# Kernel optimization log

Hardware: AMD Instinct MI355X
Metric: run time of the kernel (lower is better)

## Reference

```python
import jax, jax.numpy as jnp
import numpy as np

VOCAB, E, H = 32000, 256, 256
B, T = 64, 2048


def setup_inputs() -> dict:
    key = jax.random.key(0)
    ks = jax.random.split(key, 6)
    X = jax.random.randint(ks[0], (B, T), 0, VOCAB)
    emb = jax.random.normal(ks[1], (VOCAB, E), dtype=jnp.float32)
    W_qrnn = jax.random.normal(ks[2], (E, 3 * H), dtype=jnp.float32) / np.sqrt(E)
    b_qrnn = jnp.zeros((3 * H,), dtype=jnp.float32)
    c0 = jax.random.normal(ks[3], (B, H), dtype=jnp.float32)
    W_out = jax.random.normal(ks[4], (H, 1), dtype=jnp.float32) / np.sqrt(H)
    b_out = jnp.zeros((1,), dtype=jnp.float32)
    return {"X": X, "emb": emb, "W_qrnn": W_qrnn, "b_qrnn": b_qrnn,
            "c0": c0, "W_out": W_out, "b_out": b_out}


def reference(X, emb, W_qrnn, b_qrnn, c0, W_out, b_out):
    # Embedding lookup: [B,T] -> [B,T,E]; permute to seq-major [T,B,E]
    x = jnp.transpose(emb[X], (1, 0, 2))
    # QRNN window=1 gate projection: all timesteps in one GEMM, [T,B,3H]
    g = jnp.einsum('tbe,ef->tbf', x, W_qrnn) + b_qrnn
    z, f, o = jnp.split(g, 3, axis=-1)
    z = jnp.tanh(z)
    f = jax.nn.sigmoid(f)
    o = jax.nn.sigmoid(o)

    # fo-pooling recurrence: c_t = f_t * c_{t-1} + (1 - f_t) * z_t
    def step(c, zf):
        z_t, f_t = zf
        c = f_t * c + (1.0 - f_t) * z_t
        return c, c

    _, cs = jax.lax.scan(step, c0, (z, f))  # cs: [T,B,H]
    h = o * cs                              # h_t = o_t * c_t
    hn = h[-1]                              # last timestep, [B,H]
    return hn @ W_out + b_out               # [B,1]
```

## Files before the change

kernel.cpp:

```cpp
#include <hip/hip_runtime.h>
#include <hip/hip_bf16.h>
#include <math.h>

#define EDIM 256
#define HDIM 256
#define BDIM 64
#define TDIM 2048
#define NC   64
#define TC   32

typedef __attribute__((ext_vector_type(8)))  short  short8;
typedef __attribute__((ext_vector_type(4)))  float  floatx4;
typedef __attribute__((ext_vector_type(4)))  unsigned int uintx4;

__device__ __forceinline__ unsigned short f2bf(float f) {
    unsigned int u = __float_as_uint(f);
    u += 0x7FFFu + ((u >> 16) & 1u);
    return (unsigned short)(u >> 16);
}
__device__ __forceinline__ unsigned int pk2(float a, float b) {
    return (unsigned int)f2bf(a) | ((unsigned int)f2bf(b) << 16);
}
__device__ __forceinline__ float sigm(float x) {
    return __builtin_amdgcn_rcpf(1.f + __expf(-x));
}
__device__ __forceinline__ float tanh_fast(float x) {
    return fmaf(-2.f, __builtin_amdgcn_rcpf(1.f + __expf(2.f * x)), 1.f);
}

__global__ __launch_bounds__(256) void conv_wp(const float* __restrict__ Wq,
                                               unsigned short* __restrict__ Wp) {
    const int bx = blockIdx.x;
    const int nt = (bx >> 3) & 7;
    const int hg = bx >> 6;
    const int ks = bx & 7;
    const int t = threadIdx.x;
    const int lane = t >> 2, pj = t & 3;
    const int col = lane & 15, q = lane >> 4;
    const int h = hg * 64 + (nt & 3) * 16 + col;
    const int c = (nt < 4) ? h : (HDIM + h);
    const int k = ks * 32 + q * 8 + pj * 2;
    unsigned int v = pk2(Wq[k * (3 * HDIM) + c], Wq[(k + 1) * (3 * HDIM) + c]);
    *(unsigned int*)(Wp + (size_t)bx * 512 + lane * 8 + pj * 2) = v;
}

__global__ __launch_bounds__(256) void conv_emb(const float* __restrict__ emb,
                                                unsigned short* __restrict__ ebf) {
    size_t i = ((size_t)blockIdx.x * 256 + threadIdx.x) * 8;
    floatx4 a = *(const floatx4*)(emb + i);
    floatx4 b = *(const floatx4*)(emb + i + 4);
    uintx4 o = {pk2(a.x, a.y), pk2(a.z, a.w), pk2(b.x, b.y), pk2(b.z, b.w)};
    *(uintx4*)(ebf + i) = o;
}

template<bool EMBBF>
__global__ __launch_bounds__(256, 2) void qrnn_mfma(
    const int* __restrict__ X, const float* __restrict__ emb,
    const unsigned short* __restrict__ ebf, const unsigned short* __restrict__ Wp,
    const float* __restrict__ bq, float* __restrict__ wsA, float* __restrict__ wsB)
{
    __shared__ __align__(16) short Bs[32768];

    const int tid = threadIdx.x;
    const int chunk = blockIdx.x, bg = blockIdx.y, hg = blockIdx.z;
    const int lane = tid & 63, w = tid >> 6;
    const int col = lane & 15, q = lane >> 4;
    const int t0 = chunk * TC;

    const unsigned short* wpb = Wp + (size_t)hg * 64 * 512;
#pragma unroll
    for (int i = 0; i < 16; ++i) {
        const int ch = w * 16 + i;
        __builtin_amdgcn_global_load_lds(
            (const __attribute__((address_space(1))) unsigned int*)(wpb + ch * 512 + lane * 8),
            (__attribute__((address_space(3))) unsigned int*)(Bs + ch * 512),
            16, 0, 0);
    }

    const int b0 = bg * 8 + 2 * w;
    int xid[4];
#pragma unroll
    for (int mt = 0; mt < 4; ++mt)
        xid[mt] = X[(b0 + (mt >> 1)) * TDIM + t0 + (mt & 1) * 16 + col];

    const unsigned short* ap[4];
    const float* apf[4];
#pragma unroll
    for (int mt = 0; mt < 4; ++mt) {
        if constexpr (EMBBF) ap[mt]  = ebf + (size_t)xid[mt] * EDIM + q * 8;
        else                 apf[mt] = emb + (size_t)xid[mt] * EDIM + q * 8;
    }

    floatx4 acc[4][8];
#pragma unroll
    for (int mt = 0; mt < 4; ++mt)
#pragma unroll
        for (int nt = 0; nt < 8; ++nt) acc[mt][nt] = (floatx4){0.f, 0.f, 0.f, 0.f};

    __syncthreads();

#pragma unroll
    for (int ks = 0; ks < 8; ++ks) {
        short8 af[4];
#pragma unroll
        for (int mt = 0; mt < 4; ++mt) {
            if constexpr (EMBBF) {
                af[mt] = *(const short8*)(ap[mt] + ks * 32);
            } else {
                floatx4 f0 = *(const floatx4*)(apf[mt] + ks * 32);
                floatx4 f1 = *(const floatx4*)(apf[mt] + ks * 32 + 4);
                uintx4 p = {pk2(f0.x, f0.y), pk2(f0.z, f0.w),
                            pk2(f1.x, f1.y), pk2(f1.z, f1.w)};
                af[mt] = *(short8*)&p;
            }
        }
        short8 bf[8];
#pragma unroll
        for (int nt = 0; nt < 8; ++nt)
            bf[nt] = *(const short8*)(Bs + (nt * 8 + ks) * 512 + lane * 8);
#pragma unroll
        for (int nt = 0; nt < 8; ++nt)
#pragma unroll
            for (int mt = 0; mt < 4; ++mt)
                acc[mt][nt] = __builtin_amdgcn_mfma_f32_16x16x32_bf16(af[mt], bf[nt], acc[mt][nt], 0, 0, 0);
    }

    const int hbase = hg * 64;
    float bz[4], bff[4];
#pragma unroll
    for (int nt = 0; nt < 4; ++nt) {
        bz[nt]  = bq[hbase + nt * 16 + col];
        bff[nt] = bq[HDIM + hbase + nt * 16 + col];
    }

    float Af0[4], Bf0[4], Af1[4], Bf1[4];
#pragma unroll
    for (int nt = 0; nt < 4; ++nt) {
        float Aseg[4], Bseg[4];
#pragma unroll
        for (int mt = 0; mt < 4; ++mt) {
            float Ac = 1.f, Bc = 0.f;
#pragma unroll
            for (int j = 0; j < 4; ++j) {
                float z = tanh_fast(acc[mt][nt][j] + bz[nt]);
                float f = sigm(acc[mt][nt + 4][j] + bff[nt]);
                Ac = f * Ac;
                Bc = fmaf(f, Bc, (1.f - f) * z);
            }
            Aseg[mt] = Ac; Bseg[mt] = Bc;
        }
#pragma unroll
        for (int s = 0; s < 2; ++s) {
            const int msk = 16 << s;
            const bool self_earlier = ((q >> s) & 1) == 0;
#pragma unroll
            for (int mt = 0; mt < 4; ++mt) {
                float Ap = __shfl_xor(Aseg[mt], msk, 64);
                float Bp = __shfl_xor(Bseg[mt], msk, 64);
                Bseg[mt] = self_earlier ? fmaf(Ap, Bseg[mt], Bp)
                                        : fmaf(Aseg[mt], Bp, Bseg[mt]);
                Aseg[mt] = Aseg[mt] * Ap;
            }
        }
        Af0[nt] = Aseg[0] * Aseg[1];
        Bf0[nt] = fmaf(Aseg[1], Bseg[0], Bseg[1]);
        Af1[nt] = Aseg[2] * Aseg[3];
        Bf1[nt] = fmaf(Aseg[3], Bseg[2], Bseg[3]);
    }

    float As0 = (q == 0) ? Af0[0] : (q == 1) ? Af0[1] : (q == 2) ? Af0[2] : Af0[3];
    float Bs0 = (q == 0) ? Bf0[0] : (q == 1) ? Bf0[1] : (q == 2) ? Bf0[2] : Bf0[3];
    float As1 = (q == 0) ? Af1[0] : (q == 1) ? Af1[1] : (q == 2) ? Af1[2] : Af1[3];
    float Bs1 = (q == 0) ? Bf1[0] : (q == 1) ? Bf1[1] : (q == 2) ? Bf1[2] : Bf1[3];

    const size_t r0 = ((size_t)chunk * BDIM + b0) * HDIM + hbase + lane;
    wsA[r0] = As0;          wsB[r0] = Bs0;
    wsA[r0 + HDIM] = As1;   wsB[r0 + HDIM] = Bs1;
}

__global__ __launch_bounds__(256) void qrnn_combine(
    const float* __restrict__ wsA, const float* __restrict__ wsB,
    const float* __restrict__ c0, const int* __restrict__ X,
    const float* __restrict__ emb, const float* __restrict__ Wq,
    const float* __restrict__ bq, const float* __restrict__ Wout,
    const float* __restrict__ bout, float* __restrict__ out)
{
    const int b = blockIdx.x;
    const int h = threadIdx.x;

    float c = c0[b * HDIM + h];
    for (int c8 = 0; c8 < NC; c8 += 8) {
        float a[8], bb[8];
#pragma unroll
        for (int i = 0; i < 8; ++i) {
            size_t base = ((size_t)(c8 + i) * BDIM + b) * HDIM + h;
            a[i]  = wsA[base];
            bb[i] = wsB[base];
        }
#pragma unroll
        for (int i = 0; i < 8; ++i) c = fmaf(a[i], c, bb[i]);
    }

    __shared__ float xs[EDIM];
    int idx = X[b * TDIM + (TDIM - 1)];
    xs[h] = emb[(size_t)idx * EDIM + h];
    __syncthreads();

    float acc = 0.f;
#pragma unroll 16
    for (int e = 0; e < EDIM; ++e)
        acc = fmaf(xs[e], Wq[e * (3 * HDIM) + 2 * HDIM + h], acc);

    float o  = 1.f / (1.f + expf(-(acc + bq[2 * HDIM + h])));
    float hn = o * c;

    __shared__ float red[HDIM];
    red[h] = hn * Wout[h];
    __syncthreads();
    for (int s = HDIM / 2; s > 0; s >>= 1) {
        if (h < s) red[h] += red[h + s];
        __syncthreads();
    }
    if (h == 0) out[b] = red[0] + bout[0];
}

extern "C" void kernel_launch(void* const* d_in, const int* in_sizes, int n_in,
                              void* d_out, int out_size, void* d_ws, size_t ws_size,
                              hipStream_t stream) {
    const int*   X    = (const int*)d_in[0];
    const float* emb  = (const float*)d_in[1];
    const float* Wq   = (const float*)d_in[2];
    const float* bq   = (const float*)d_in[3];
    const float* c0   = (const float*)d_in[4];
    const float* Wout = (const float*)d_in[5];
    const float* bout = (const float*)d_in[6];
    float* out = (float*)d_out;

    float* wsA = (float*)d_ws;
    float* wsB = wsA + (size_t)NC * BDIM * HDIM;
    unsigned short* Wp  = (unsigned short*)(wsB + (size_t)NC * BDIM * HDIM);
    unsigned short* ebf = Wp + (size_t)256 * 512;

    const size_t need_full = (size_t)2 * NC * BDIM * HDIM * 4
                           + (size_t)256 * 512 * 2
                           + (size_t)32000 * EDIM * 2;
    const bool full = ws_size >= need_full;

    conv_wp<<<256, 256, 0, stream>>>(Wq, Wp);
    if (full)
        conv_emb<<<(32000 * EDIM / 8) / 256, 256, 0, stream>>>(emb, ebf);

    dim3 g(NC, BDIM / 8, HDIM / 64);
    if (full) qrnn_mfma<true ><<<g, 256, 0, stream>>>(X, emb, ebf, Wp, bq, wsA, wsB);
    else      qrnn_mfma<false><<<g, 256, 0, stream>>>(X, emb, ebf, Wp, bq, wsA, wsB);

    qrnn_combine<<<BDIM, 256, 0, stream>>>(wsA, wsB, c0, X, emb, Wq, bq, Wout, bout, out);
}
```

Measured before the change: 169.4 us.

## Process multiple time chunks per block with prefetched A fragments and merged pack kernel

New measurement: 150.0 us. 11.5% less time.

```diff
diff --git a/kernel.cpp b/kernel.cpp
--- a/kernel.cpp
+++ b/kernel.cpp
@@ -8,6 +8,7 @@
 #define TDIM 2048
 #define NC   64
 #define TC   32
+#define CPB  4
 
 typedef __attribute__((ext_vector_type(8)))  short  short8;
 typedef __attribute__((ext_vector_type(4)))  float  floatx4;
@@ -28,29 +29,30 @@
     return fmaf(-2.f, __builtin_amdgcn_rcpf(1.f + __expf(2.f * x)), 1.f);
 }
 
-__global__ __launch_bounds__(256) void conv_wp(const float* __restrict__ Wq,
-                                               unsigned short* __restrict__ Wp) {
+__global__ __launch_bounds__(256) void qrnn_pack(
+    const float* __restrict__ Wq, const float* __restrict__ emb,
+    unsigned short* __restrict__ Wp, unsigned short* __restrict__ ebf)
+{
     const int bx = blockIdx.x;
-    const int nt = (bx >> 3) & 7;
-    const int hg = bx >> 6;
-    const int ks = bx & 7;
-    const int t = threadIdx.x;
-    const int lane = t >> 2, pj = t & 3;
-    const int col = lane & 15, q = lane >> 4;
-    const int h = hg * 64 + (nt & 3) * 16 + col;
-    const int c = (nt < 4) ? h : (HDIM + h);
-    const int k = ks * 32 + q * 8 + pj * 2;
-    unsigned int v = pk2(Wq[k * (3 * HDIM) + c], Wq[(k + 1) * (3 * HDIM) + c]);
-    *(unsigned int*)(Wp + (size_t)bx * 512 + lane * 8 + pj * 2) = v;
-}
-
-__global__ __launch_bounds__(256) void conv_emb(const float* __restrict__ emb,
-                                                unsigned short* __restrict__ ebf) {
-    size_t i = ((size_t)blockIdx.x * 256 + threadIdx.x) * 8;
-    floatx4 a = *(const floatx4*)(emb + i);
-    floatx4 b = *(const floatx4*)(emb + i + 4);
-    uintx4 o = {pk2(a.x, a.y), pk2(a.z, a.w), pk2(b.x, b.y), pk2(b.z, b.w)};
-    *(uintx4*)(ebf + i) = o;
+    if (bx < 256) {
+        const int nt = (bx >> 3) & 7;
+        const int hg = bx >> 6;
+        const int ks = bx & 7;
+        const int t = threadIdx.x;
+        const int lane = t >> 2, pj = t & 3;
+        const int col = lane & 15, q = lane >> 4;
+        const int h = hg * 64 + (nt & 3) * 16 + col;
+        const int c = (nt < 4) ? h : (HDIM + h);
+        const int k = ks * 32 + q * 8 + pj * 2;
+        unsigned int v = pk2(Wq[k * (3 * HDIM) + c], Wq[(k + 1) * (3 * HDIM) + c]);
+        *(unsigned int*)(Wp + (size_t)bx * 512 + lane * 8 + pj * 2) = v;
+    } else {
+        size_t i = ((size_t)(bx - 256) * 256 + threadIdx.x) * 8;
+        floatx4 a = *(const floatx4*)(emb + i);
+        floatx4 b = *(const floatx4*)(emb + i + 4);
+        uintx4 o = {pk2(a.x, a.y), pk2(a.z, a.w), pk2(b.x, b.y), pk2(b.z, b.w)};
+        *(uintx4*)(ebf + i) = o;
+    }
 }
 
 template<bool EMBBF>
@@ -59,71 +61,30 @@
     const unsigned short* __restrict__ ebf, const unsigned short* __restrict__ Wp,
     const float* __restrict__ bq, float* __restrict__ wsA, float* __restrict__ wsB)
 {
-    __shared__ __align__(16) short Bs[32768];
+    __shared__ __align__(16) short Bsh[32768];
 
     const int tid = threadIdx.x;
-    const int chunk = blockIdx.x, bg = blockIdx.y, hg = blockIdx.z;
+    const int cg = blockIdx.x, bg = blockIdx.y, hg = blockIdx.z;
     const int lane = tid & 63, w = tid >> 6;
     const int col = lane & 15, q = lane >> 4;
-    const int t0 = chunk * TC;
-
-    const unsigned short* wpb = Wp + (size_t)hg * 64 * 512;
+
+    const unsigned short* wpb = Wp + (size_t)hg * 32768;
 #pragma unroll
     for (int i = 0; i < 16; ++i) {
         const int ch = w * 16 + i;
         __builtin_amdgcn_global_load_lds(
             (const __attribute__((address_space(1))) unsigned int*)(wpb + ch * 512 + lane * 8),
-            (__attribute__((address_space(3))) unsigned int*)(Bs + ch * 512),
+            (__attribute__((address_space(3))) unsigned int*)(Bsh + ch * 512),
             16, 0, 0);
     }
 
     const int b0 = bg * 8 + 2 * w;
-    int xid[4];
-#pragma unroll
-    for (int mt = 0; mt < 4; ++mt)
-        xid[mt] = X[(b0 + (mt >> 1)) * TDIM + t0 + (mt & 1) * 16 + col];
-
-    const unsigned short* ap[4];
-    const float* apf[4];
-#pragma unroll
-    for (int mt = 0; mt < 4; ++mt) {
-        if constexpr (EMBBF) ap[mt]  = ebf + (size_t)xid[mt] * EDIM + q * 8;
-        else                 apf[mt] = emb + (size_t)xid[mt] * EDIM + q * 8;
-    }
-
-    floatx4 acc[4][8];
-#pragma unroll
-    for (int mt = 0; mt < 4; ++mt)
-#pragma unroll
-        for (int nt = 0; nt < 8; ++nt) acc[mt][nt] = (floatx4){0.f, 0.f, 0.f, 0.f};
-
-    __syncthreads();
-
-#pragma unroll
-    for (int ks = 0; ks < 8; ++ks) {
-        short8 af[4];
-#pragma unroll
-        for (int mt = 0; mt < 4; ++mt) {
-            if constexpr (EMBBF) {
-                af[mt] = *(const short8*)(ap[mt] + ks * 32);
-            } else {
-                floatx4 f0 = *(const floatx4*)(apf[mt] + ks * 32);
-                floatx4 f1 = *(const floatx4*)(apf[mt] + ks * 32 + 4);
-                uintx4 p = {pk2(f0.x, f0.y), pk2(f0.z, f0.w),
-                            pk2(f1.x, f1.y), pk2(f1.z, f1.w)};
-                af[mt] = *(short8*)&p;
-            }
-        }
-        short8 bf[8];
-#pragma unroll
-        for (int nt = 0; nt < 8; ++nt)
-            bf[nt] = *(const short8*)(Bs + (nt * 8 + ks) * 512 + lane * 8);
-#pragma unroll
-        for (int nt = 0; nt < 8; ++nt)
-#pragma unroll
-            for (int mt = 0; mt < 4; ++mt)
-                acc[mt][nt] = __builtin_amdgcn_mfma_f32_16x16x32_bf16(af[mt], bf[nt], acc[mt][nt], 0, 0, 0);
-    }
+    int xid[CPB][4];
+#pragma unroll
+    for (int c = 0; c < CPB; ++c)
+#pragma unroll
+        for (int mt = 0; mt < 4; ++mt)
+            xid[c][mt] = X[(b0 + (mt >> 1)) * TDIM + (cg * CPB + c) * TC + (mt & 1) * 16 + col];
 
     const int hbase = hg * 64;
     float bz[4], bff[4];
@@ -133,49 +94,102 @@
         bff[nt] = bq[HDIM + hbase + nt * 16 + col];
     }
 
-    float Af0[4], Bf0[4], Af1[4], Bf1[4];
-#pragma unroll
-    for (int nt = 0; nt < 4; ++nt) {
-        float Aseg[4], Bseg[4];
+    short8 abuf[3][4];
+    auto fetchA = [&](int c, int ks, int slot) {
 #pragma unroll
         for (int mt = 0; mt < 4; ++mt) {
-            float Ac = 1.f, Bc = 0.f;
-#pragma unroll
-            for (int j = 0; j < 4; ++j) {
-                float z = tanh_fast(acc[mt][nt][j] + bz[nt]);
-                float f = sigm(acc[mt][nt + 4][j] + bff[nt]);
-                Ac = f * Ac;
-                Bc = fmaf(f, Bc, (1.f - f) * z);
+            if constexpr (EMBBF) {
+                abuf[slot][mt] = *(const short8*)(ebf + (size_t)xid[c][mt] * EDIM + q * 8 + ks * 32);
+            } else {
+                const float* ap = emb + (size_t)xid[c][mt] * EDIM + q * 8 + ks * 32;
+                floatx4 f0 = *(const floatx4*)ap;
+                floatx4 f1 = *(const floatx4*)(ap + 4);
+                uintx4 p = {pk2(f0.x, f0.y), pk2(f0.z, f0.w),
+                            pk2(f1.x, f1.y), pk2(f1.z, f1.w)};
+                abuf[slot][mt] = *(short8*)&p;
             }
-            Aseg[mt] = Ac; Bseg[mt] = Bc;
-        }
-#pragma unroll
-        for (int s = 0; s < 2; ++s) {
-            const int msk = 16 << s;
-            const bool self_earlier = ((q >> s) & 1) == 0;
+        }
+    };
+
+    floatx4 acc[4][8];
+#pragma unroll
+    for (int mt = 0; mt < 4; ++mt)
+#pragma unroll
+        for (int nt = 0; nt < 8; ++nt) acc[mt][nt] = (floatx4){0.f, 0.f, 0.f, 0.f};
+
+    fetchA(0, 0, 0);
+    fetchA(0, 1, 1);
+    __syncthreads();
+
+#pragma unroll
+    for (int c = 0; c < CPB; ++c) {
+#pragma unroll
+        for (int ks = 0; ks < 8; ++ks) {
+            const int s = c * 8 + ks;
+            if (s + 2 < CPB * 8)
+                fetchA((s + 2) >> 3, (s + 2) & 7, (s + 2) % 3);
+            short8 bf[8];
+#pragma unroll
+            for (int nt = 0; nt < 8; ++nt)
+                bf[nt] = *(const short8*)(Bsh + (nt * 8 + ks) * 512 + lane * 8);
+            const int sl = s % 3;
+#pragma unroll
+            for (int nt = 0; nt < 8; ++nt)
+#pragma unroll
+                for (int mt = 0; mt < 4; ++mt)
+                    acc[mt][nt] = __builtin_amdgcn_mfma_f32_16x16x32_bf16(abuf[sl][mt], bf[nt], acc[mt][nt], 0, 0, 0);
+        }
+
+        const int cc = cg * CPB + c;
+        float Af0[4], Bf0[4], Af1[4], Bf1[4];
+#pragma unroll
+        for (int nt = 0; nt < 4; ++nt) {
+            float Aseg[4], Bseg[4];
 #pragma unroll
             for (int mt = 0; mt < 4; ++mt) {
-                float Ap = __shfl_xor(Aseg[mt], msk, 64);
-                float Bp = __shfl_xor(Bseg[mt], msk, 64);
-                Bseg[mt] = self_earlier ? fmaf(Ap, Bseg[mt], Bp)
-                                        : fmaf(Aseg[mt], Bp, Bseg[mt]);
-                Aseg[mt] = Aseg[mt] * Ap;
+                float Ac = 1.f, Bc = 0.f;
+#pragma unroll
+                for (int j = 0; j < 4; ++j) {
+                    float z = tanh_fast(acc[mt][nt][j] + bz[nt]);
+                    float f = sigm(acc[mt][nt + 4][j] + bff[nt]);
+                    Ac = f * Ac;
+                    Bc = fmaf(f, Bc, (1.f - f) * z);
+                }
+                Aseg[mt] = Ac; Bseg[mt] = Bc;
             }
-        }
-        Af0[nt] = Aseg[0] * Aseg[1];
-        Bf0[nt] = fmaf(Aseg[1], Bseg[0], Bseg[1]);
-        Af1[nt] = Aseg[2] * Aseg[3];
-        Bf1[nt] = fmaf(Aseg[3], Bseg[2], Bseg[3]);
-    }
-
-    float As0 = (q == 0) ? Af0[0] : (q == 1) ? Af0[1] : (q == 2) ? Af0[2] : Af0[3];
-    float Bs0 = (q == 0) ? Bf0[0] : (q == 1) ? Bf0[1] : (q == 2) ? Bf0[2] : Bf0[3];
-    float As1 = (q == 0) ? Af1[0] : (q == 1) ? Af1[1] : (q == 2) ? Af1[2] : Af1[3];
-    float Bs1 = (q == 0) ? Bf1[0] : (q == 1) ? Bf1[1] : (q == 2) ? Bf1[2] : Bf1[3];
-
-    const size_t r0 = ((size_t)chunk * BDIM + b0) * HDIM + hbase + lane;
-    wsA[r0] = As0;          wsB[r0] = Bs0;
-    wsA[r0 + HDIM] = As1;   wsB[r0 + HDIM] = Bs1;
+#pragma unroll
+            for (int st = 0; st < 2; ++st) {
+                const int msk = 16 << st;
+                const bool self_earlier = ((q >> st) & 1) == 0;
+#pragma unroll
+                for (int mt = 0; mt < 4; ++mt) {
+                    float Ap = __shfl_xor(Aseg[mt], msk, 64);
+                    float Bp = __shfl_xor(Bseg[mt], msk, 64);
+                    Bseg[mt] = self_earlier ? fmaf(Ap, Bseg[mt], Bp)
+                                            : fmaf(Aseg[mt], Bp, Bseg[mt]);
+                    Aseg[mt] = Aseg[mt] * Ap;
+                }
+            }
+            Af0[nt] = Aseg[0] * Aseg[1];
+            Bf0[nt] = fmaf(Aseg[1], Bseg[0], Bseg[1]);
+            Af1[nt] = Aseg[2] * Aseg[3];
+            Bf1[nt] = fmaf(Aseg[3], Bseg[2], Bseg[3]);
+        }
+
+        float As0 = (q == 0) ? Af0[0] : (q == 1) ? Af0[1] : (q == 2) ? Af0[2] : Af0[3];
+        float Bs0 = (q == 0) ? Bf0[0] : (q == 1) ? Bf0[1] : (q == 2) ? Bf0[2] : Bf0[3];
+        float As1 = (q == 0) ? Af1[0] : (q == 1) ? Af1[1] : (q == 2) ? Af1[2] : Af1[3];
+        float Bs1 = (q == 0) ? Bf1[0] : (q == 1) ? Bf1[1] : (q == 2) ? Bf1[2] : Bf1[3];
+
+        const size_t r0 = ((size_t)cc * BDIM + b0) * HDIM + hbase + lane;
+        wsA[r0] = As0;          wsB[r0] = Bs0;
+        wsA[r0 + HDIM] = As1;   wsB[r0 + HDIM] = Bs1;
+
+#pragma unroll
+        for (int mt = 0; mt < 4; ++mt)
+#pragma unroll
+            for (int nt = 0; nt < 8; ++nt) acc[mt][nt] = (floatx4){0.f, 0.f, 0.f, 0.f};
+    }
 }
 
 __global__ __launch_bounds__(256) void qrnn_combine(
@@ -246,11 +260,10 @@
                            + (size_t)32000 * EDIM * 2;
     const bool full = ws_size >= need_full;
 
-    conv_wp<<<256, 256, 0, stream>>>(Wq, Wp);
-    if (full)
-        conv_emb<<<(32000 * EDIM / 8) / 256, 256, 0, stream>>>(emb, ebf);
-
-    dim3 g(NC, BDIM / 8, HDIM / 64);
+    const int emb_blocks = (32000 * EDIM / 8) / 256;
+    qrnn_pack<<<256 + (full ? emb_blocks : 0), 256, 0, stream>>>(Wq, emb, Wp, ebf);
+
+    dim3 g(NC / CPB, BDIM / 8, HDIM / 64);
     if (full) qrnn_mfma<true ><<<g, 256, 0, stream>>>(X, emb, ebf, Wp, bq, wsA, wsB);
     else      qrnn_mfma<false><<<g, 256, 0, stream>>>(X, emb, ebf, Wp, bq, wsA, wsB);
 
```
